# Kernel optimization log

Measured on AMD Instinct MI355X. Metric: run time of the kernel, lower is better.

The kernel has to match this reference:

```python
import jax, jax.numpy as jnp
import numpy as np

EPS = 1e-5
GROUPS = 32


def group_norm(x, w, b):
    # x: [N, C]; GroupNorm over 1x1 spatial == per-group norm over C//GROUPS chans
    N, C = x.shape
    xg = x.reshape(N, GROUPS, C // GROUPS)
    mu = xg.mean(-1, keepdims=True)
    var = xg.var(-1, keepdims=True)
    xn = ((xg - mu) * jax.lax.rsqrt(var + EPS)).reshape(N, C)
    return xn * w + b


def rb(x, gn1w, gn1b, c1w, c1b, gn2w, gn2b, c2w, c2b):
    # Conv2d 3x3 pad=1 on a 1x1 spatial input: only the center tap sees data
    # (all other taps hit zero padding), so it reduces exactly to a GEMM with
    # the [out, in] center slice of the kernel.
    h = jax.nn.silu(group_norm(x, gn1w, gn1b))
    h = h @ c1w[:, :, 1, 1].T + c1b
    h = jax.nn.silu(group_norm(h, gn2w, gn2b))
    h = h @ c2w[:, :, 1, 1].T + c2b
    return h + x  # skip == Identity (in_ch == out_ch)


def setup_inputs() -> dict:
    key = jax.random.key(0)
    ks = jax.random.split(key, 20)
    BS, CAND, D, H, W = 32, 2048, 256, 32, 32
    s = 0.05
    inp = {
        "gimage": jax.random.normal(ks[0], (BS, D, H, W), dtype=jnp.float32),
        "pts": jax.random.randint(ks[1], (BS, CAND, 1, 2), 0, 256, dtype=jnp.int32),
        # two stacked RB blocks
        "gn1_w": jnp.ones((2, D), jnp.float32),
        "gn1_b": jnp.zeros((2, D), jnp.float32),
        "conv1_w": jax.random.normal(ks[2], (2, D, D, 3, 3), jnp.float32) * s,
        "conv1_b": jnp.zeros((2, D), jnp.float32),
        "gn2_w": jnp.ones((2, D), jnp.float32),
        "gn2_b": jnp.zeros((2, D), jnp.float32),
        "conv2_w": jax.random.normal(ks[3], (2, D, D, 3, 3), jnp.float32) * s,
        "conv2_b": jnp.zeros((2, D), jnp.float32),
        # class_embed: Linear(256, 2)
        "cls_w": jax.random.normal(ks[4], (2, D), jnp.float32) * s,
        "cls_b": jnp.zeros((2,), jnp.float32),
        # bbox_embed: MLP(256, 256, 4, 3)
        "mlp_w1": jax.random.normal(ks[5], (D, D), jnp.float32) * s,
        "mlp_b1": jnp.zeros((D,), jnp.float32),
        "mlp_w2": jax.random.normal(ks[6], (D, D), jnp.float32) * s,
        "mlp_b2": jnp.zeros((D,), jnp.float32),
        "mlp_w3": jax.random.normal(ks[7], (4, D), jnp.float32) * s,
        "mlp_b3": jnp.zeros((4,), jnp.float32),
    }
    return inp


def reference(gimage, pts, gn1_w, gn1_b, conv1_w, conv1_b, gn2_w, gn2_b,
              conv2_w, conv2_b, cls_w, cls_b, mlp_w1, mlp_b1, mlp_w2, mlp_b2,
              mlp_w3, mlp_b3):
    bs, C, H, W = gimage.shape
    c = pts.shape[1]
    # patch_idx = (pts // 8)[:, :, 0, :] -> (iy, ix) per (batch, candidate)
    idx = pts[:, :, 0, :] // 8                      # [bs, c, 2]
    lin = idx[..., 0] * W + idx[..., 1]             # [bs, c] flat spatial index
    g = gimage.reshape(bs, C, H * W)
    feat = jnp.take_along_axis(g, lin[:, None, :].astype(jnp.int32), axis=2)  # [bs, C, c]
    x = feat.transpose(0, 2, 1).reshape(bs * c, C)  # [(bs c), 256]

    for i in range(2):  # convLayer = Sequential(RB, RB)
        x = rb(x, gn1_w[i], gn1_b[i], conv1_w[i], conv1_b[i],
               gn2_w[i], gn2_b[i], conv2_w[i], conv2_b[i])

    logits = x @ cls_w.T + cls_b                    # [(bs c), 2]
    h = jax.nn.relu(x @ mlp_w1.T + mlp_b1)
    h = jax.nn.relu(h @ mlp_w2.T + mlp_b2)
    boxes = jax.nn.sigmoid(h @ mlp_w3.T + mlp_b3)   # [(bs c), 4]

    pred_logits = logits.reshape(bs, c, 2)
    pred_boxes = boxes.reshape(bs, c, 4)
    return pred_logits, pred_boxes
```

## Files before the change

### kernel.cpp

```cpp
#include <hip/hip_runtime.h>


typedef __attribute__((ext_vector_type(8))) _Float16 half8;
typedef __attribute__((ext_vector_type(4))) float f32x4;

#define AS 264

#define NHALF  393216
#define OFF_WC1 0
#define OFF_WC2 131072
#define OFF_W1  262144
#define OFF_W2  327680
#define WS_NEED 1572864

__device__ __forceinline__ float sigm(float y) { return 1.f / (1.f + __expf(-y)); }

template <int CTRL>
__device__ __forceinline__ float dppadd(float v) {
  union { float f; int i; } u, r;
  u.f = v;
  r.i = __builtin_amdgcn_update_dpp(0, u.i, CTRL, 0xf, 0xf, true);
  return v + r.f;
}
#define DPP_X1 0xB1
#define DPP_X2 0x4E
#define DPP_X7 0x141
#define DPP_XF 0x140

__device__ __forceinline__ float gsum8(float v) {
  v = dppadd<DPP_X1>(v);
  v = dppadd<DPP_X2>(v);
  v = dppadd<DPP_X7>(v);
  return v;
}
__device__ __forceinline__ float gsum16(float v) {
  v = dppadd<DPP_X1>(v);
  v = dppadd<DPP_X2>(v);
  v = dppadd<DPP_X7>(v);
  v = dppadd<DPP_XF>(v);
  return v;
}

__global__ __launch_bounds__(256) void prep(const float* __restrict__ c1w,
                                            const float* __restrict__ c2w,
                                            const float* __restrict__ w1,
                                            const float* __restrict__ w2,
                                            _Float16* __restrict__ ws) {
  int i = blockIdx.x * 256 + threadIdx.x;
  {
    float v = c1w[(size_t)i * 9 + 4];
    _Float16 h = (_Float16)v;
    ws[OFF_WC1 + i] = h;
    ws[NHALF + OFF_WC1 + i] = (_Float16)(v - (float)h);
  }
  {
    float v = c2w[(size_t)i * 9 + 4];
    _Float16 h = (_Float16)v;
    ws[OFF_WC2 + i] = h;
    ws[NHALF + OFF_WC2 + i] = (_Float16)(v - (float)h);
  }
  if (i < 65536) {
    float v = w1[i];
    _Float16 h = (_Float16)v;
    ws[OFF_W1 + i] = h;
    ws[NHALF + OFF_W1 + i] = (_Float16)(v - (float)h);
    v = w2[i];
    h = (_Float16)v;
    ws[OFF_W2 + i] = h;
    ws[NHALF + OFF_W2 + i] = (_Float16)(v - (float)h);
  }
}

__device__ __forceinline__ void hl_store(_Float16* __restrict__ Ah,
                                         _Float16* __restrict__ Al,
                                         int idx, float v) {
  _Float16 h = (_Float16)v;
  Ah[idx] = h;
  Al[idx] = (_Float16)(v - (float)h);
}

struct BF { half8 h[4], l[4]; };

__device__ __forceinline__ void preloadB(BF& B,
    const _Float16* __restrict__ Wh, const _Float16* __restrict__ Wl,
    size_t boff) {
  #pragma unroll
  for (int nt = 0; nt < 4; nt++) {
    B.h[nt] = *(const half8*)(Wh + boff + (nt << 12));
    B.l[nt] = *(const half8*)(Wl + boff + (nt << 12));
  }
}

__device__ __forceinline__ void mfma_body(f32x4 acc[2][4], BF& B,
    const _Float16* __restrict__ Ah, const _Float16* __restrict__ Al,
    const _Float16* __restrict__ Wh, const _Float16* __restrict__ Wl,
    int aoff, size_t boff) {
  #pragma unroll
  for (int mt = 0; mt < 2; mt++)
    #pragma unroll
    for (int nt = 0; nt < 4; nt++)
      acc[mt][nt] = (f32x4){0.f, 0.f, 0.f, 0.f};
  __syncthreads();
  #pragma unroll
  for (int kt = 0; kt < 8; kt++) {
    half8 ah0 = *(const half8*)(Ah + aoff + kt * 32);
    half8 ah1 = *(const half8*)(Ah + aoff + 16 * AS + kt * 32);
    half8 al0 = *(const half8*)(Al + aoff + kt * 32);
    half8 al1 = *(const half8*)(Al + aoff + 16 * AS + kt * 32);
    #pragma unroll
    for (int nt = 0; nt < 4; nt++) {
      acc[0][nt] = __builtin_amdgcn_mfma_f32_16x16x32_f16(ah0, B.h[nt], acc[0][nt], 0, 0, 0);
      acc[1][nt] = __builtin_amdgcn_mfma_f32_16x16x32_f16(ah1, B.h[nt], acc[1][nt], 0, 0, 0);
      acc[0][nt] = __builtin_amdgcn_mfma_f32_16x16x32_f16(ah0, B.l[nt], acc[0][nt], 0, 0, 0);
      acc[1][nt] = __builtin_amdgcn_mfma_f32_16x16x32_f16(ah1, B.l[nt], acc[1][nt], 0, 0, 0);
      acc[0][nt] = __builtin_amdgcn_mfma_f32_16x16x32_f16(al0, B.h[nt], acc[0][nt], 0, 0, 0);
      acc[1][nt] = __builtin_amdgcn_mfma_f32_16x16x32_f16(al1, B.h[nt], acc[1][nt], 0, 0, 0);
    }
    if (kt < 7) {
      #pragma unroll
      for (int nt = 0; nt < 4; nt++) {
        B.h[nt] = *(const half8*)(Wh + boff + (nt << 12) + (kt + 1) * 32);
        B.l[nt] = *(const half8*)(Wl + boff + (nt << 12) + (kt + 1) * 32);
      }
    }
  }
}

__device__ __forceinline__ void gn_x_to_A(const float x[2][4][4],
    const float* __restrict__ gnw, const float* __restrict__ gnb,
    int col, int quad, int nb,
    _Float16* __restrict__ Ah, _Float16* __restrict__ Al) {
  #pragma unroll
  for (int nt = 0; nt < 4; nt++) {
    int n = nb + (nt << 4) + col;
    float gwv = gnw[n], gbv = gnb[n];
    #pragma unroll
    for (int mt = 0; mt < 2; mt++) {
      #pragma unroll
      for (int rg = 0; rg < 4; rg++) {
        float v = x[mt][nt][rg];
        float s = gsum8(v);
        float q = gsum8(v * v);
        float mu = s * 0.125f;
        float rs = rsqrtf(q * 0.125f - mu * mu + 1e-5f);
        float y = (v - mu) * rs * gwv + gbv;
        float sv = y * sigm(y);
        hl_store(Ah, Al, ((mt << 4) + (quad << 2) + rg) * AS + n, sv);
      }
    }
  }
}

__device__ __forceinline__ void epi_gn_to_A(const f32x4 acc[2][4],
    const float* __restrict__ bias,
    const float* __restrict__ gnw, const float* __restrict__ gnb,
    int col, int quad, int nb,
    _Float16* __restrict__ Ah, _Float16* __restrict__ Al) {
  #pragma unroll
  for (int nt = 0; nt < 4; nt++) {
    int n = nb + (nt << 4) + col;
    float bv = bias[n];
    float gwv = gnw[n], gbv = gnb[n];
    #pragma unroll
    for (int mt = 0; mt < 2; mt++) {
      #pragma unroll
      for (int rg = 0; rg < 4; rg++) {
        float v = acc[mt][nt][rg] + bv;
        float s = gsum8(v);
        float q = gsum8(v * v);
        float mu = s * 0.125f;
        float rs = rsqrtf(q * 0.125f - mu * mu + 1e-5f);
        float y = (v - mu) * rs * gwv + gbv;
        float sv = y * sigm(y);
        hl_store(Ah, Al, ((mt << 4) + (quad << 2) + rg) * AS + n, sv);
      }
    }
  }
}

__device__ __forceinline__ void epi_relu_to_A(const f32x4 acc[2][4],
    const float* __restrict__ bias, int col, int quad, int nb,
    _Float16* __restrict__ Ah, _Float16* __restrict__ Al) {
  #pragma unroll
  for (int nt = 0; nt < 4; nt++) {
    int n = nb + (nt << 4) + col;
    float bv = bias[n];
    #pragma unroll
    for (int mt = 0; mt < 2; mt++)
      #pragma unroll
      for (int rg = 0; rg < 4; rg++)
        hl_store(Ah, Al, ((mt << 4) + (quad << 2) + rg) * AS + n,
                 fmaxf(acc[mt][nt][rg] + bv, 0.f));
  }
}

__global__ __launch_bounds__(256, 3) void fused_mfma(
    const float* __restrict__ gimage, const int* __restrict__ pts,
    const float* __restrict__ gn1w, const float* __restrict__ gn1b,
    const float* __restrict__ c1b,
    const float* __restrict__ gn2w, const float* __restrict__ gn2b,
    const float* __restrict__ c2b,
    const float* __restrict__ clsw, const float* __restrict__ clsb,
    const float* __restrict__ b1, const float* __restrict__ b2,
    const float* __restrict__ w3, const float* __restrict__ b3,
    const _Float16* __restrict__ ws, float* __restrict__ out) {
  __shared__ _Float16 Ah[32 * AS];
  __shared__ _Float16 Al[32 * AS];
  __shared__ float red[4][32][4];

  const int t = threadIdx.x;
  const int w = t >> 6;
  const int lane = t & 63;
  const int col = lane & 15;
  const int quad = lane >> 4;
  const int nb = w << 6;
  const int bsw = ((blockIdx.x & 7) << 8) | (blockIdx.x >> 3);
  const int row0 = bsw << 5;
  const int rbase = quad << 2;

  const int aoff = col * AS + (quad << 3);
  const size_t boff = (((size_t)(nb + col)) << 8) + (quad << 3);
  const _Float16* wsl = ws + NHALF;

  float x[2][4][4];
  {
    int lin[2][4];
    #pragma unroll
    for (int mt = 0; mt < 2; mt++)
      #pragma unroll
      for (int rg = 0; rg < 4; rg++) {
        int grow = row0 + (mt << 4) + rbase + rg;
        int p0 = pts[2 * grow], p1 = pts[2 * grow + 1];
        lin[mt][rg] = ((p0 >> 3) << 5) + (p1 >> 3);
      }
    const float* gbase = gimage + (((size_t)((row0 >> 11) << 8)) << 10);
    #pragma unroll
    for (int nt = 0; nt < 4; nt++) {
      const float* gc = gbase + (((size_t)(nb + (nt << 4) + col)) << 10);
      #pragma unroll
      for (int mt = 0; mt < 2; mt++)
        #pragma unroll
        for (int rg = 0; rg < 4; rg++)
          x[mt][nt][rg] = gc[lin[mt][rg]];
    }
  }

  f32x4 acc[2][4];
  BF B;

  preloadB(B, ws + OFF_WC1, wsl + OFF_WC1, boff);
  #pragma unroll 1
  for (int rb = 0; rb < 2; rb++) {
    gn_x_to_A(x, gn1w + (rb << 8), gn1b + (rb << 8), col, quad, nb, Ah, Al);
    mfma_body(acc, B, Ah, Al, ws + OFF_WC1 + (rb << 16),
              wsl + OFF_WC1 + (rb << 16), aoff, boff);
    __syncthreads();
    preloadB(B, ws + OFF_WC2 + (rb << 16), wsl + OFF_WC2 + (rb << 16), boff);
    epi_gn_to_A(acc, c1b + (rb << 8), gn2w + (rb << 8), gn2b + (rb << 8),
                col, quad, nb, Ah, Al);
    mfma_body(acc, B, Ah, Al, ws + OFF_WC2 + (rb << 16),
              wsl + OFF_WC2 + (rb << 16), aoff, boff);
    __syncthreads();
    if (rb == 0)
      preloadB(B, ws + OFF_WC1 + 65536, wsl + OFF_WC1 + 65536, boff);
    else
      preloadB(B, ws + OFF_W1, wsl + OFF_W1, boff);
    #pragma unroll
    for (int nt = 0; nt < 4; nt++) {
      float bv = c2b[(rb << 8) + nb + (nt << 4) + col];
      #pragma unroll
      for (int mt = 0; mt < 2; mt++)
        #pragma unroll
        for (int rg = 0; rg < 4; rg++)
          x[mt][nt][rg] += acc[mt][nt][rg] + bv;
    }
  }

  #pragma unroll
  for (int nt = 0; nt < 4; nt++) {
    int n = nb + (nt << 4) + col;
    #pragma unroll
    for (int mt = 0; mt < 2; mt++)
      #pragma unroll
      for (int rg = 0; rg < 4; rg++)
        hl_store(Ah, Al, ((mt << 4) + rbase + rg) * AS + n, x[mt][nt][rg]);
  }
  {
    float pc[2][2][4];
    #pragma unroll
    for (int j = 0; j < 2; j++) {
      #pragma unroll
      for (int mt = 0; mt < 2; mt++)
        #pragma unroll
        for (int rg = 0; rg < 4; rg++)
          pc[j][mt][rg] = 0.f;
      #pragma unroll
      for (int nt = 0; nt < 4; nt++) {
        float wv = clsw[(j << 8) + nb + (nt << 4) + col];
        #pragma unroll
        for (int mt = 0; mt < 2; mt++)
          #pragma unroll
          for (int rg = 0; rg < 4; rg++)
            pc[j][mt][rg] += x[mt][nt][rg] * wv;
      }
    }
    #pragma unroll
    for (int j = 0; j < 2; j++)
      #pragma unroll
      for (int mt = 0; mt < 2; mt++)
        #pragma unroll
        for (int rg = 0; rg < 4; rg++) {
          float p = gsum16(pc[j][mt][rg]);
          if (col == 0) red[w][(mt << 4) + rbase + rg][j] = p;
        }
  }

  mfma_body(acc, B, Ah, Al, ws + OFF_W1, wsl + OFF_W1, aoff, boff);
  if (t < 64) {
    int r = t >> 1, j = t & 1;
    out[((size_t)(row0 + r) << 1) + j] =
        clsb[j] + red[0][r][j] + red[1][r][j] + red[2][r][j] + red[3][r][j];
  }
  __syncthreads();
  preloadB(B, ws + OFF_W2, wsl + OFF_W2, boff);
  epi_relu_to_A(acc, b1, col, quad, nb, Ah, Al);

  mfma_body(acc, B, Ah, Al, ws + OFF_W2, wsl + OFF_W2, aoff, boff);
  __syncthreads();
  {
    float pb[4][2][4];
    #pragma unroll
    for (int j = 0; j < 4; j++)
      #pragma unroll
      for (int mt = 0; mt < 2; mt++)
        #pragma unroll
        for (int rg = 0; rg < 4; rg++)
          pb[j][mt][rg] = 0.f;
    #pragma unroll
    for (int nt = 0; nt < 4; nt++) {
      int n = nb + (nt << 4) + col;
      float bv = b2[n];
      float w0 = w3[n], w1v = w3[256 + n], w2v = w3[512 + n], w3v = w3[768 + n];
      #pragma unroll
      for (int mt = 0; mt < 2; mt++)
        #pragma unroll
        for (int rg = 0; rg < 4; rg++) {
          float v = fmaxf(acc[mt][nt][rg] + bv, 0.f);
          pb[0][mt][rg] += v * w0;
          pb[1][mt][rg] += v * w1v;
          pb[2][mt][rg] += v * w2v;
          pb[3][mt][rg] += v * w3v;
        }
    }
    #pragma unroll
    for (int j = 0; j < 4; j++)
      #pragma unroll
      for (int mt = 0; mt < 2; mt++)
        #pragma unroll
        for (int rg = 0; rg < 4; rg++) {
          float p = gsum16(pb[j][mt][rg]);
          if (col == 0) red[w][(mt << 4) + rbase + rg][j] = p;
        }
  }
  __syncthreads();
  if (t < 128) {
    int r = t >> 2, j = t & 3;
    float s = b3[j] + red[0][r][j] + red[1][r][j] + red[2][r][j] + red[3][r][j];
    out[131072 + ((size_t)(row0 + r) << 2) + j] = sigm(s);
  }
}

#define LS 260
template <int EPI, bool CONV>
__device__ __forceinline__ void gemm_f32(const float* __restrict__ src,
                                         const float* __restrict__ W,
                                         const float* __restrict__ bias,
                                         float* __restrict__ dst,
                                         float* __restrict__ X) {
  const int n = threadIdx.x;
  float acc[32];
  #pragma unroll
  for (int r = 0; r < 32; r++) acc[r] = 0.f;
  #pragma unroll 1
  for (int k = 0; k < 256; k += 8) {
    float w[8];
    if (CONV) {
      #pragma unroll
      for (int j = 0; j < 8; j++) w[j] = W[(size_t)((n << 8) + k + j) * 9 + 4];
    } else {
      f32x4 wa = *(const f32x4*)(W + (n << 8) + k);
      f32x4 wb = *(const f32x4*)(W + (n << 8) + k + 4);
      w[0] = wa[0]; w[1] = wa[1]; w[2] = wa[2]; w[3] = wa[3];
      w[4] = wb[0]; w[5] = wb[1]; w[6] = wb[2]; w[7] = wb[3];
    }
    #pragma unroll
    for (int r = 0; r < 32; r++) {
      const float* xr = src + r * LS + k;
      f32x4 a0 = *(const f32x4*)xr, a1 = *(const f32x4*)(xr + 4);
      acc[r] += a0[0] * w[0] + a0[1] * w[1] + a0[2] * w[2] + a0[3] * w[3]
              + a1[0] * w[4] + a1[1] * w[5] + a1[2] * w[6] + a1[3] * w[7];
    }
  }
  float bv = bias[n];
  #pragma unroll
  for (int r = 0; r < 32; r++) {
    float v = acc[r] + bv;
    if (EPI == 0) dst[r * LS + n] = v;
    else if (EPI == 1) X[r * LS + n] += v;
    else dst[r * LS + n] = fmaxf(v, 0.f);
  }
}
__device__ __forceinline__ void gn_silu32(const float* __restrict__ src,
                                          float* __restrict__ dst,
                                          const float* __restrict__ gw,
                                          const float* __restrict__ gb, int t) {
  #pragma unroll
  for (int i = 0; i < 4; i++) {
    int task = (i << 8) + t;
    int r = task >> 5, g = task & 31;
    const float* x = src + r * LS + (g << 3);
    f32x4 x0 = *(const f32x4*)x, x1 = *(const f32x4*)(x + 4);
    float xx[8] = {x0[0], x0[1], x0[2], x0[3], x1[0], x1[1], x1[2], x1[3]};
    float s = 0.f, q = 0.f;
    #pragma unroll
    for (int j = 0; j < 8; j++) { s += xx[j]; q += xx[j] * xx[j]; }
    float mu = s * 0.125f;
    float rs = rsqrtf(q * 0.125f - mu * mu + 1e-5f);
    const float* w = gw + (g << 3);
    const float* b = gb + (g << 3);
    float* d = dst + r * LS + (g << 3);
    #pragma unroll
    for (int j = 0; j < 8; j++) {
      float y = (xx[j] - mu) * rs * w[j] + b[j];
      d[j] = y * sigm(y);
    }
  }
}
__global__ __launch_bounds__(256, 1) void fused_all(
    const float* __restrict__ gimage, const int* __restrict__ pts,
    const float* __restrict__ gn1w, const float* __restrict__ gn1b,
    const float* __restrict__ c1w, const float* __restrict__ c1b,
    const float* __restrict__ gn2w, const float* __restrict__ gn2b,
    const float* __restrict__ c2w, const float* __restrict__ c2b,
    const float* __restrict__ clsw, const float* __restrict__ clsb,
    const float* __restrict__ w1, const float* __restrict__ b1,
    const float* __restrict__ w2, const float* __restrict__ b2,
    const float* __restrict__ w3, const float* __restrict__ b3,
    float* __restrict__ out) {
  __shared__ float X[32 * LS];
  __shared__ float A[32 * LS];
  __shared__ float H[32 * LS];
  const int t = threadIdx.x;
  const int row0 = blockIdx.x << 5;
  {
    int r = t >> 3;
    int c0 = (t & 7) << 5;
    int grow = row0 + r;
    int p0 = pts[2 * grow], p1 = pts[2 * grow + 1];
    int lin = ((p0 >> 3) << 5) + (p1 >> 3);
    int b = grow >> 11;
    const float* src = gimage + (((size_t)((b << 8) + c0)) << 10) + lin;
    #pragma unroll
    for (int c = 0; c < 32; c++) X[r * LS + c0 + c] = src[(size_t)c << 10];
  }
  __syncthreads();
  #pragma unroll 1
  for (int rb = 0; rb < 2; rb++) {
    gn_silu32(X, A, gn1w + (rb << 8), gn1b + (rb << 8), t);
    __syncthreads();
    gemm_f32<0, true>(A, c1w + rb * 589824, c1b + (rb << 8), H, nullptr);
    __syncthreads();
    gn_silu32(H, A, gn2w + (rb << 8), gn2b + (rb << 8), t);
    __syncthreads();
    gemm_f32<1, true>(A, c2w + rb * 589824, c2b + (rb << 8), nullptr, X);
    __syncthreads();
  }
  if (t < 64) {
    int r = t >> 1, j = t & 1;
    float s = clsb[j];
    const float* w = clsw + (j << 8);
    const float* x = X + r * LS;
    #pragma unroll 1
    for (int k = 0; k < 256; k += 4) {
      f32x4 wv = *(const f32x4*)(w + k);
      f32x4 xv = *(const f32x4*)(x + k);
      s += xv[0] * wv[0] + xv[1] * wv[1] + xv[2] * wv[2] + xv[3] * wv[3];
    }
    out[((size_t)(row0 + r) << 1) + j] = s;
  }
  gemm_f32<2, false>(X, w1, b1, H, nullptr);
  __syncthreads();
  gemm_f32<2, false>(H, w2, b2, A, nullptr);
  __syncthreads();
  if (t < 128) {
    int r = t >> 2, j = t & 3;
    float s = b3[j];
    const float* w = w3 + (j << 8);
    const float* x = A + r * LS;
    #pragma unroll 1
    for (int k = 0; k < 256; k += 4) {
      f32x4 wv = *(const f32x4*)(w + k);
      f32x4 xv = *(const f32x4*)(x + k);
      s += xv[0] * wv[0] + xv[1] * wv[1] + xv[2] * wv[2] + xv[3] * wv[3];
    }
    out[131072 + ((size_t)(row0 + r) << 2) + j] = sigm(s);
  }
}

extern "C" void kernel_launch(void* const* d_in, const int* in_sizes, int n_in,
                              void* d_out, int out_size, void* d_ws, size_t ws_size,
                              hipStream_t stream) {
  const float* gimage = (const float*)d_in[0];
  const int* pts = (const int*)d_in[1];
  const float* gn1w = (const float*)d_in[2];
  const float* gn1b = (const float*)d_in[3];
  const float* c1w = (const float*)d_in[4];
  const float* c1b = (const float*)d_in[5];
  const float* gn2w = (const float*)d_in[6];
  const float* gn2b = (const float*)d_in[7];
  const float* c2w = (const float*)d_in[8];
  const float* c2b = (const float*)d_in[9];
  const float* clsw = (const float*)d_in[10];
  const float* clsb = (const float*)d_in[11];
  const float* w1 = (const float*)d_in[12];
  const float* b1 = (const float*)d_in[13];
  const float* w2 = (const float*)d_in[14];
  const float* b2 = (const float*)d_in[15];
  const float* w3 = (const float*)d_in[16];
  const float* b3 = (const float*)d_in[17];

  if (ws_size >= (size_t)WS_NEED) {
    _Float16* ws = (_Float16*)d_ws;
    prep<<<512, 256, 0, stream>>>(c1w, c2w, w1, w2, ws);
    fused_mfma<<<2048, 256, 0, stream>>>(gimage, pts, gn1w, gn1b, c1b,
                                         gn2w, gn2b, c2b, clsw, clsb,
                                         b1, b2, w3, b3, ws, (float*)d_out);
  } else {
    fused_all<<<2048, 256, 0, stream>>>(gimage, pts, gn1w, gn1b, c1w, c1b,
                                        gn2w, gn2b, c2w, c2b, clsw, clsb,
                                        w1, b1, w2, b2, w3, b3, (float*)d_out);
  }
}
```

Baseline: 494.8 us.

## Process two 32-row tiles per block to reuse B-fragment weight loads

Each block now handles 64 rows as two 32-row tiles, with separate LDS A buffers and accumulators per tile. A dual MFMA body shares each loaded weight fragment across both tiles, halving global weight traffic per row. The grid is halved and launch bounds drop to 2 waves per SIMD, since register and LDS use roughly double. This trades occupancy and latency hiding for more MFMA work per weight load.

```diff
diff --git a/kernel.cpp b/kernel.cpp
--- a/kernel.cpp
+++ b/kernel.cpp
@@ -91,31 +91,66 @@
   }
 }
 
-__device__ __forceinline__ void mfma_body(f32x4 acc[2][4], BF& B,
-    const _Float16* __restrict__ Ah, const _Float16* __restrict__ Al,
+__device__ __forceinline__ void mfma_dual(f32x4 accA[2][4], f32x4 accB[2][4],
+    BF& B,
+    const _Float16* __restrict__ AhA, const _Float16* __restrict__ AlA,
+    const _Float16* __restrict__ AhB, const _Float16* __restrict__ AlB,
     const _Float16* __restrict__ Wh, const _Float16* __restrict__ Wl,
     int aoff, size_t boff) {
   #pragma unroll
   for (int mt = 0; mt < 2; mt++)
     #pragma unroll
-    for (int nt = 0; nt < 4; nt++)
-      acc[mt][nt] = (f32x4){0.f, 0.f, 0.f, 0.f};
+    for (int nt = 0; nt < 4; nt++) {
+      accA[mt][nt] = (f32x4){0.f, 0.f, 0.f, 0.f};
+      accB[mt][nt] = (f32x4){0.f, 0.f, 0.f, 0.f};
+    }
   __syncthreads();
   #pragma unroll
   for (int kt = 0; kt < 8; kt++) {
-    half8 ah0 = *(const half8*)(Ah + aoff + kt * 32);
-    half8 ah1 = *(const half8*)(Ah + aoff + 16 * AS + kt * 32);
-    half8 al0 = *(const half8*)(Al + aoff + kt * 32);
-    half8 al1 = *(const half8*)(Al + aoff + 16 * AS + kt * 32);
-    #pragma unroll
-    for (int nt = 0; nt < 4; nt++) {
-      acc[0][nt] = __builtin_amdgcn_mfma_f32_16x16x32_f16(ah0, B.h[nt], acc[0][nt], 0, 0, 0);
-      acc[1][nt] = __builtin_amdgcn_mfma_f32_16x16x32_f16(ah1, B.h[nt], acc[1][nt], 0, 0, 0);
-      acc[0][nt] = __builtin_amdgcn_mfma_f32_16x16x32_f16(ah0, B.l[nt], acc[0][nt], 0, 0, 0);
-      acc[1][nt] = __builtin_amdgcn_mfma_f32_16x16x32_f16(ah1, B.l[nt], acc[1][nt], 0, 0, 0);
-      acc[0][nt] = __builtin_amdgcn_mfma_f32_16x16x32_f16(al0, B.h[nt], acc[0][nt], 0, 0, 0);
-      acc[1][nt] = __builtin_amdgcn_mfma_f32_16x16x32_f16(al1, B.h[nt], acc[1][nt], 0, 0, 0);
-    }
+    half8 a0hA = *(const half8*)(AhA + aoff + kt * 32);
+    half8 a1hA = *(const half8*)(AhA + aoff + 16 * AS + kt * 32);
+    half8 a0lA = *(const half8*)(AlA + aoff + kt * 32);
+    half8 a1lA = *(const half8*)(AlA + aoff + 16 * AS + kt * 32);
+    half8 a0hB = *(const half8*)(AhB + aoff + kt * 32);
+    half8 a1hB = *(const half8*)(AhB + aoff + 16 * AS + kt * 32);
+    half8 a0lB = *(const half8*)(AlB + aoff + kt * 32);
+    half8 a1lB = *(const half8*)(AlB + aoff + 16 * AS + kt * 32);
+    #pragma unroll
+    for (int nt = 0; nt < 4; nt++)
+      accA[0][nt] = __builtin_amdgcn_mfma_f32_16x16x32_f16(a0hA, B.h[nt], accA[0][nt], 0, 0, 0);
+    #pragma unroll
+    for (int nt = 0; nt < 4; nt++)
+      accB[0][nt] = __builtin_amdgcn_mfma_f32_16x16x32_f16(a0hB, B.h[nt], accB[0][nt], 0, 0, 0);
+    #pragma unroll
+    for (int nt = 0; nt < 4; nt++)
+      accA[1][nt] = __builtin_amdgcn_mfma_f32_16x16x32_f16(a1hA, B.h[nt], accA[1][nt], 0, 0, 0);
+    #pragma unroll
+    for (int nt = 0; nt < 4; nt++)
+      accB[1][nt] = __builtin_amdgcn_mfma_f32_16x16x32_f16(a1hB, B.h[nt], accB[1][nt], 0, 0, 0);
+    #pragma unroll
+    for (int nt = 0; nt < 4; nt++)
+      accA[0][nt] = __builtin_amdgcn_mfma_f32_16x16x32_f16(a0hA, B.l[nt], accA[0][nt], 0, 0, 0);
+    #pragma unroll
+    for (int nt = 0; nt < 4; nt++)
+      accB[0][nt] = __builtin_amdgcn_mfma_f32_16x16x32_f16(a0hB, B.l[nt], accB[0][nt], 0, 0, 0);
+    #pragma unroll
+    for (int nt = 0; nt < 4; nt++)
+      accA[1][nt] = __builtin_amdgcn_mfma_f32_16x16x32_f16(a1hA, B.l[nt], accA[1][nt], 0, 0, 0);
+    #pragma unroll
+    for (int nt = 0; nt < 4; nt++)
+      accB[1][nt] = __builtin_amdgcn_mfma_f32_16x16x32_f16(a1hB, B.l[nt], accB[1][nt], 0, 0, 0);
+    #pragma unroll
+    for (int nt = 0; nt < 4; nt++)
+      accA[0][nt] = __builtin_amdgcn_mfma_f32_16x16x32_f16(a0lA, B.h[nt], accA[0][nt], 0, 0, 0);
+    #pragma unroll
+    for (int nt = 0; nt < 4; nt++)
+      accB[0][nt] = __builtin_amdgcn_mfma_f32_16x16x32_f16(a0lB, B.h[nt], accB[0][nt], 0, 0, 0);
+    #pragma unroll
+    for (int nt = 0; nt < 4; nt++)
+      accA[1][nt] = __builtin_amdgcn_mfma_f32_16x16x32_f16(a1lA, B.h[nt], accA[1][nt], 0, 0, 0);
+    #pragma unroll
+    for (int nt = 0; nt < 4; nt++)
+      accB[1][nt] = __builtin_amdgcn_mfma_f32_16x16x32_f16(a1lB, B.h[nt], accB[1][nt], 0, 0, 0);
     if (kt < 7) {
       #pragma unroll
       for (int nt = 0; nt < 4; nt++) {
@@ -194,7 +229,31 @@
   }
 }
 
-__global__ __launch_bounds__(256, 3) void fused_mfma(
+__device__ __forceinline__ void gatherX(float x[2][4][4],
+    const float* __restrict__ gimage, const int* __restrict__ pts,
+    int tbase, int rbase, int nb, int col) {
+  int lin[2][4];
+  #pragma unroll
+  for (int mt = 0; mt < 2; mt++)
+    #pragma unroll
+    for (int rg = 0; rg < 4; rg++) {
+      int grow = tbase + (mt << 4) + rbase + rg;
+      int p0 = pts[2 * grow], p1 = pts[2 * grow + 1];
+      lin[mt][rg] = ((p0 >> 3) << 5) + (p1 >> 3);
+    }
+  const float* gbase = gimage + (((size_t)((tbase >> 11) << 8)) << 10);
+  #pragma unroll
+  for (int nt = 0; nt < 4; nt++) {
+    const float* gc = gbase + (((size_t)(nb + (nt << 4) + col)) << 10);
+    #pragma unroll
+    for (int mt = 0; mt < 2; mt++)
+      #pragma unroll
+      for (int rg = 0; rg < 4; rg++)
+        x[mt][nt][rg] = gc[lin[mt][rg]];
+  }
+}
+
+__global__ __launch_bounds__(256, 2) void fused_mfma(
     const float* __restrict__ gimage, const int* __restrict__ pts,
     const float* __restrict__ gn1w, const float* __restrict__ gn1b,
     const float* __restrict__ c1b,
@@ -204,9 +263,9 @@
     const float* __restrict__ b1, const float* __restrict__ b2,
     const float* __restrict__ w3, const float* __restrict__ b3,
     const _Float16* __restrict__ ws, float* __restrict__ out) {
-  __shared__ _Float16 Ah[32 * AS];
-  __shared__ _Float16 Al[32 * AS];
-  __shared__ float red[4][32][4];
+  __shared__ _Float16 AhA[32 * AS], AlA[32 * AS];
+  __shared__ _Float16 AhB[32 * AS], AlB[32 * AS];
+  __shared__ float red[4][64][4];
 
   const int t = threadIdx.x;
   const int w = t >> 6;
@@ -214,52 +273,38 @@
   const int col = lane & 15;
   const int quad = lane >> 4;
   const int nb = w << 6;
-  const int bsw = ((blockIdx.x & 7) << 8) | (blockIdx.x >> 3);
-  const int row0 = bsw << 5;
+  const int bsw = ((blockIdx.x & 7) << 7) | (blockIdx.x >> 3);
+  const int row0 = bsw << 6;
   const int rbase = quad << 2;
 
   const int aoff = col * AS + (quad << 3);
   const size_t boff = (((size_t)(nb + col)) << 8) + (quad << 3);
   const _Float16* wsl = ws + NHALF;
 
-  float x[2][4][4];
-  {
-    int lin[2][4];
-    #pragma unroll
-    for (int mt = 0; mt < 2; mt++)
-      #pragma unroll
-      for (int rg = 0; rg < 4; rg++) {
-        int grow = row0 + (mt << 4) + rbase + rg;
-        int p0 = pts[2 * grow], p1 = pts[2 * grow + 1];
-        lin[mt][rg] = ((p0 >> 3) << 5) + (p1 >> 3);
-      }
-    const float* gbase = gimage + (((size_t)((row0 >> 11) << 8)) << 10);
-    #pragma unroll
-    for (int nt = 0; nt < 4; nt++) {
-      const float* gc = gbase + (((size_t)(nb + (nt << 4) + col)) << 10);
-      #pragma unroll
-      for (int mt = 0; mt < 2; mt++)
-        #pragma unroll
-        for (int rg = 0; rg < 4; rg++)
-          x[mt][nt][rg] = gc[lin[mt][rg]];
-    }
-  }
-
-  f32x4 acc[2][4];
+  float xA[2][4][4], xB[2][4][4];
+  gatherX(xA, gimage, pts, row0, rbase, nb, col);
+  gatherX(xB, gimage, pts, row0 + 32, rbase, nb, col);
+
+  f32x4 accA[2][4], accB[2][4];
   BF B;
 
   preloadB(B, ws + OFF_WC1, wsl + OFF_WC1, boff);
   #pragma unroll 1
   for (int rb = 0; rb < 2; rb++) {
-    gn_x_to_A(x, gn1w + (rb << 8), gn1b + (rb << 8), col, quad, nb, Ah, Al);
-    mfma_body(acc, B, Ah, Al, ws + OFF_WC1 + (rb << 16),
-              wsl + OFF_WC1 + (rb << 16), aoff, boff);
+    gn_x_to_A(xA, gn1w + (rb << 8), gn1b + (rb << 8), col, quad, nb, AhA, AlA);
+    gn_x_to_A(xB, gn1w + (rb << 8), gn1b + (rb << 8), col, quad, nb, AhB, AlB);
+    mfma_dual(accA, accB, B, AhA, AlA, AhB, AlB,
+              ws + OFF_WC1 + (rb << 16), wsl + OFF_WC1 + (rb << 16),
+              aoff, boff);
     __syncthreads();
     preloadB(B, ws + OFF_WC2 + (rb << 16), wsl + OFF_WC2 + (rb << 16), boff);
-    epi_gn_to_A(acc, c1b + (rb << 8), gn2w + (rb << 8), gn2b + (rb << 8),
-                col, quad, nb, Ah, Al);
-    mfma_body(acc, B, Ah, Al, ws + OFF_WC2 + (rb << 16),
-              wsl + OFF_WC2 + (rb << 16), aoff, boff);
+    epi_gn_to_A(accA, c1b + (rb << 8), gn2w + (rb << 8), gn2b + (rb << 8),
+                col, quad, nb, AhA, AlA);
+    epi_gn_to_A(accB, c1b + (rb << 8), gn2w + (rb << 8), gn2b + (rb << 8),
+                col, quad, nb, AhB, AlB);
+    mfma_dual(accA, accB, B, AhA, AlA, AhB, AlB,
+              ws + OFF_WC2 + (rb << 16), wsl + OFF_WC2 + (rb << 16),
+              aoff, boff);
     __syncthreads();
     if (rb == 0)
       preloadB(B, ws + OFF_WC1 + 65536, wsl + OFF_WC1 + 65536, boff);
@@ -271,8 +316,10 @@
       #pragma unroll
       for (int mt = 0; mt < 2; mt++)
         #pragma unroll
-        for (int rg = 0; rg < 4; rg++)
-          x[mt][nt][rg] += acc[mt][nt][rg] + bv;
+        for (int rg = 0; rg < 4; rg++) {
+          xA[mt][nt][rg] += accA[mt][nt][rg] + bv;
+          xB[mt][nt][rg] += accB[mt][nt][rg] + bv;
+        }
     }
   }
 
@@ -282,8 +329,10 @@
     #pragma unroll
     for (int mt = 0; mt < 2; mt++)
       #pragma unroll
-      for (int rg = 0; rg < 4; rg++)
-        hl_store(Ah, Al, ((mt << 4) + rbase + rg) * AS + n, x[mt][nt][rg]);
+      for (int rg = 0; rg < 4; rg++) {
+        hl_store(AhA, AlA, ((mt << 4) + rbase + rg) * AS + n, xA[mt][nt][rg]);
+        hl_store(AhB, AlB, ((mt << 4) + rbase + rg) * AS + n, xB[mt][nt][rg]);
+      }
   }
   {
     float pc[2][2][4];
@@ -301,7 +350,7 @@
         for (int mt = 0; mt < 2; mt++)
           #pragma unroll
           for (int rg = 0; rg < 4; rg++)
-            pc[j][mt][rg] += x[mt][nt][rg] * wv;
+            pc[j][mt][rg] += xA[mt][nt][rg] * wv;
       }
     }
     #pragma unroll
@@ -313,19 +362,48 @@
           float p = gsum16(pc[j][mt][rg]);
           if (col == 0) red[w][(mt << 4) + rbase + rg][j] = p;
         }
-  }
-
-  mfma_body(acc, B, Ah, Al, ws + OFF_W1, wsl + OFF_W1, aoff, boff);
-  if (t < 64) {
+    #pragma unroll
+    for (int j = 0; j < 2; j++) {
+      #pragma unroll
+      for (int mt = 0; mt < 2; mt++)
+        #pragma unroll
+        for (int rg = 0; rg < 4; rg++)
+          pc[j][mt][rg] = 0.f;
+      #pragma unroll
+      for (int nt = 0; nt < 4; nt++) {
+        float wv = clsw[(j << 8) + nb + (nt << 4) + col];
+        #pragma unroll
+        for (int mt = 0; mt < 2; mt++)
+          #pragma unroll
+          for (int rg = 0; rg < 4; rg++)
+            pc[j][mt][rg] += xB[mt][nt][rg] * wv;
+      }
+    }
+    #pragma unroll
+    for (int j = 0; j < 2; j++)
+      #pragma unroll
+      for (int mt = 0; mt < 2; mt++)
+        #pragma unroll
+        for (int rg = 0; rg < 4; rg++) {
+          float p = gsum16(pc[j][mt][rg]);
+          if (col == 0) red[w][32 + (mt << 4) + rbase + rg][j] = p;
+        }
+  }
+
+  mfma_dual(accA, accB, B, AhA, AlA, AhB, AlB,
+            ws + OFF_W1, wsl + OFF_W1, aoff, boff);
+  if (t < 128) {
     int r = t >> 1, j = t & 1;
     out[((size_t)(row0 + r) << 1) + j] =
         clsb[j] + red[0][r][j] + red[1][r][j] + red[2][r][j] + red[3][r][j];
   }
   __syncthreads();
   preloadB(B, ws + OFF_W2, wsl + OFF_W2, boff);
-  epi_relu_to_A(acc, b1, col, quad, nb, Ah, Al);
-
-  mfma_body(acc, B, Ah, Al, ws + OFF_W2, wsl + OFF_W2, aoff, boff);
+  epi_relu_to_A(accA, b1, col, quad, nb, AhA, AlA);
+  epi_relu_to_A(accB, b1, col, quad, nb, AhB, AlB);
+
+  mfma_dual(accA, accB, B, AhA, AlA, AhB, AlB,
+            ws + OFF_W2, wsl + OFF_W2, aoff, boff);
   __syncthreads();
   {
     float pb[4][2][4];
@@ -345,7 +423,7 @@
       for (int mt = 0; mt < 2; mt++)
         #pragma unroll
         for (int rg = 0; rg < 4; rg++) {
-          float v = fmaxf(acc[mt][nt][rg] + bv, 0.f);
+          float v = fmaxf(accA[mt][nt][rg] + bv, 0.f);
           pb[0][mt][rg] += v * w0;
           pb[1][mt][rg] += v * w1v;
           pb[2][mt][rg] += v * w2v;
@@ -361,9 +439,41 @@
           float p = gsum16(pb[j][mt][rg]);
           if (col == 0) red[w][(mt << 4) + rbase + rg][j] = p;
         }
+    #pragma unroll
+    for (int j = 0; j < 4; j++)
+      #pragma unroll
+      for (int mt = 0; mt < 2; mt++)
+        #pragma unroll
+        for (int rg = 0; rg < 4; rg++)
+          pb[j][mt][rg] = 0.f;
+    #pragma unroll
+    for (int nt = 0; nt < 4; nt++) {
+      int n = nb + (nt << 4) + col;
+      float bv = b2[n];
+      float w0 = w3[n], w1v = w3[256 + n], w2v = w3[512 + n], w3v = w3[768 + n];
+      #pragma unroll
+      for (int mt = 0; mt < 2; mt++)
+        #pragma unroll
+        for (int rg = 0; rg < 4; rg++) {
+          float v = fmaxf(accB[mt][nt][rg] + bv, 0.f);
+          pb[0][mt][rg] += v * w0;
+          pb[1][mt][rg] += v * w1v;
+          pb[2][mt][rg] += v * w2v;
+          pb[3][mt][rg] += v * w3v;
+        }
+    }
+    #pragma unroll
+    for (int j = 0; j < 4; j++)
+      #pragma unroll
+      for (int mt = 0; mt < 2; mt++)
+        #pragma unroll
+        for (int rg = 0; rg < 4; rg++) {
+          float p = gsum16(pb[j][mt][rg]);
+          if (col == 0) red[w][32 + (mt << 4) + rbase + rg][j] = p;
+        }
   }
   __syncthreads();
-  if (t < 128) {
+  {
     int r = t >> 2, j = t & 3;
     float s = b3[j] + red[0][r][j] + red[1][r][j] + red[2][r][j] + red[3][r][j];
     out[131072 + ((size_t)(row0 + r) << 2) + j] = sigm(s);
@@ -532,7 +642,7 @@
   if (ws_size >= (size_t)WS_NEED) {
     _Float16* ws = (_Float16*)d_ws;
     prep<<<512, 256, 0, stream>>>(c1w, c2w, w1, w2, ws);
-    fused_mfma<<<2048, 256, 0, stream>>>(gimage, pts, gn1w, gn1b, c1b,
+    fused_mfma<<<1024, 256, 0, stream>>>(gimage, pts, gn1w, gn1b, c1b,
                                          gn2w, gn2b, c2b, clsw, clsb,
                                          b1, b2, w3, b3, ws, (float*)d_out);
   } else {
```

Measured after the change: 451.9 us. -8.7%, faster.
